# Performance work log

Hardware: AMD Instinct MI355X
Metric: run time of the kernel (lower is better)

Reference implementation:

```python
import jax, jax.numpy as jnp
import numpy as np

H_IMG, W_IMG = 256, 512      # image_size
P = 224                      # focus_patch_size
FS = 14                      # feature_size -> L = 196
DM = 384                     # d_model
POOL = P // FS               # 16


def _grid_sample_bilinear_zeros(img, grid):
    """torch F.grid_sample(mode='bilinear', padding_mode='zeros', align_corners=False).
    img: (B, C, H, W), grid: (B, Ho, Wo, 2) with (x, y) in [-1, 1]. -> (B, C, Ho, Wo)"""
    B, C, H, W = img.shape
    ix = (grid[..., 0] + 1.0) * (W * 0.5) - 0.5
    iy = (grid[..., 1] + 1.0) * (H * 0.5) - 0.5
    x0 = jnp.floor(ix); y0 = jnp.floor(iy)
    x1 = x0 + 1.0;      y1 = y0 + 1.0
    wx1 = ix - x0; wx0 = 1.0 - wx1
    wy1 = iy - y0; wy0 = 1.0 - wy1

    def gather(im, yy, xx):
        valid = ((xx >= 0) & (xx < W) & (yy >= 0) & (yy < H)).astype(im.dtype)
        xc = jnp.clip(xx, 0, W - 1).astype(jnp.int32)
        yc = jnp.clip(yy, 0, H - 1).astype(jnp.int32)
        return im[:, yc, xc] * valid[None]  # (C, Ho, Wo)

    def sample_one(im, x0, x1, y0, y1, wx0, wx1, wy0, wy1):
        return (gather(im, y0, x0) * (wy0 * wx0)[None]
                + gather(im, y0, x1) * (wy0 * wx1)[None]
                + gather(im, y1, x0) * (wy1 * wx0)[None]
                + gather(im, y1, x1) * (wy1 * wx1)[None])

    return jax.vmap(sample_one)(img, x0, x1, y0, y1, wx0, wx1, wy0, wy1)


def setup_inputs() -> dict:
    key = jax.random.key(0)
    ks = jax.random.split(key, 9)
    B = 128
    images = jax.random.normal(ks[0], (B, 3, H_IMG, W_IMG), jnp.float32)
    positions = jax.random.uniform(ks[1], (B, 2), jnp.float32)          # (x, y) in [0,1]
    global_features = jax.random.normal(ks[2], (B, FS * FS, DM), jnp.float32)
    Wp = jax.random.normal(ks[3], (3, DM), jnp.float32) * 0.1           # focus_net stand-in proj
    bp = jnp.zeros((DM,), jnp.float32)
    w1 = jax.random.normal(ks[4], (DM, DM // 4), jnp.float32) * 0.05    # fusion-weight MLP
    b1 = jnp.zeros((DM // 4,), jnp.float32)
    w2 = jax.random.normal(ks[5], (DM // 4, 1), jnp.float32) * 0.05
    b2 = jnp.zeros((1,), jnp.float32)
    return dict(images=images, positions=positions, global_features=global_features,
                Wp=Wp, bp=bp, w1=w1, b1=b1, w2=w2, b2=b2, seq_len=1)


def reference(images, positions, global_features, Wp, bp, w1, b1, w2, b2, seq_len):
    B = images.shape[0]
    L = FS * FS
    # ---- get_img_patches: wraparound crop (vectorized over batch) ----
    px = jnp.clip(positions[:, 0], 0.0, 1.0)
    py = jnp.clip(positions[:, 1], 0.0, 1.0)
    x_start = (jnp.trunc(px * W_IMG - P / 2).astype(jnp.int32)) % W_IMG           # int() then % W
    y_start = jnp.floor(jnp.clip(py * H_IMG - P / 2, 0.0, H_IMG - P)).astype(jnp.int32)
    xi = (x_start[:, None] + jnp.arange(P)[None, :]) % W_IMG                      # (B, P) wraparound
    yi = y_start[:, None] + jnp.arange(P)[None, :]                                # (B, P)
    patches = jax.vmap(lambda im, y, x: im[:, y][:, :, x])(images, yi, xi)        # (B, 3, P, P)

    # affine_grid(theta, (1,1,FS,FS), align_corners=False)
    xs = x_start.astype(jnp.float32)
    ys = y_start.astype(jnp.float32)
    u = ((jnp.arange(FS, dtype=jnp.float32) + 0.5) * 2.0 / FS) - 1.0              # base grid coords
    gx = (P / W_IMG) * u[None, None, :] + ((2.0 * xs + P) / W_IMG - 1.0)[:, None, None]
    gy = (P / H_IMG) * u[None, :, None] + ((2.0 * ys + P) / H_IMG - 1.0)[:, None, None]
    grid = jnp.stack([jnp.broadcast_to(gx, (B, FS, FS)),
                      jnp.broadcast_to(gy, (B, FS, FS))], axis=-1)                # (B, FS, FS, 2)

    # ---- focus_net stand-in: 16x16 avg-pool + linear 3 -> d_model ----
    pooled = patches.reshape(B, 3, FS, POOL, FS, POOL).mean(axis=(3, 5))          # (B, 3, FS, FS)
    local = jnp.einsum('bchw,cd->bhwd', pooled, Wp) + bp                          # (B, FS, FS, DM)
    local_features = local.reshape(B, L, DM)

    # ---- update_global_features: grid_sample scatter + gated update ----
    local_2d = local.transpose(0, 3, 1, 2)                                        # (B, DM, FS, FS)
    fw = jax.nn.sigmoid(jnp.einsum('blk,ko->blo',
                                   jax.nn.gelu(jnp.einsum('blc,ch->blh', local_features, w1) + b1),
                                   w2) + b2)                                      # (B, L, 1)
    sampled = _grid_sample_bilinear_zeros(local_2d, grid)                         # (B, DM, FS, FS)
    sampled = sampled.transpose(0, 2, 3, 1).reshape(B, L, DM)
    updated = global_features + fw * sampled                                      # broadcast expand
    return updated
```

## Files before the change

kernel.cpp:

```cpp
#include <hip/hip_runtime.h>
#include <math.h>

#define H_IMG 256
#define W_IMG 512
#define PSZ   224
#define FS    14
#define L     196
#define DM    384
#define HID   96
#define TPB   32

__device__ __forceinline__ void get_starts(const float* __restrict__ pos, int b,
                                           int& xs, int& ys) {
    float px = pos[b * 2 + 0];
    float py = pos[b * 2 + 1];
    px = fminf(fmaxf(px, 0.0f), 1.0f);
    py = fminf(fmaxf(py, 0.0f), 1.0f);
    int xv = (int)truncf(px * (float)W_IMG - 112.0f);
    xs = ((xv % W_IMG) + W_IMG) % W_IMG;
    float yv = py * (float)H_IMG - 112.0f;
    yv = fminf(fmaxf(yv, 0.0f), (float)(H_IMG - PSZ));
    ys = (int)floorf(yv);
}

__global__ __launch_bounds__(256) void pool_pre_kernel(
    const float* __restrict__ img, const float* __restrict__ pos,
    const float* __restrict__ Wp,  const float* __restrict__ bp,
    const float* __restrict__ w1,  const float* __restrict__ b1,
    float* __restrict__ pooled, float* __restrict__ A, float* __restrict__ B0,
    int B)
{
    const int HW = H_IMG * W_IMG;
    int blk = blockIdx.x;
    int b = blk / FS;
    int i = blk % FS;
    int t = threadIdx.x;
    int xs, ys;
    get_starts(pos, b, xs, ys);

    if (t < PSZ) {
        int col = xs + t;
        if (col >= W_IMG) col -= W_IMG;
        int row0 = ys + i * 16;
        const float* ip = img + (size_t)b * 3 * HW + (size_t)row0 * W_IMG + col;
        float a0 = 0.f, a1 = 0.f, a2 = 0.f;
        #pragma unroll
        for (int dy = 0; dy < 16; ++dy) {
            const float* r = ip + dy * W_IMG;
            a0 += r[0];
            a1 += r[HW];
            a2 += r[2 * HW];
        }
        #pragma unroll
        for (int d = 1; d < 16; d <<= 1) {
            a0 += __shfl_xor(a0, d);
            a1 += __shfl_xor(a1, d);
            a2 += __shfl_xor(a2, d);
        }
        if ((t & 15) == 0) {
            int li = i * FS + (t >> 4);
            pooled[((size_t)b * 3 + 0) * L + li] = a0 * (1.0f / 256.0f);
            pooled[((size_t)b * 3 + 1) * L + li] = a1 * (1.0f / 256.0f);
            pooled[((size_t)b * 3 + 2) * L + li] = a2 * (1.0f / 256.0f);
        }
    }

    if (blk == 0 && t < HID) {
        float a0 = 0.f, a1 = 0.f, a2 = 0.f, ab = 0.f;
        #pragma unroll 4
        for (int d = 0; d < DM; ++d) {
            float w = w1[d * HID + t];
            a0 += Wp[0 * DM + d] * w;
            a1 += Wp[1 * DM + d] * w;
            a2 += Wp[2 * DM + d] * w;
            ab += bp[d] * w;
        }
        A[0 * HID + t] = a0;
        A[1 * HID + t] = a1;
        A[2 * HID + t] = a2;
        B0[t] = ab + b1[t];
    }
}

__global__ __launch_bounds__(256) void fused_update_kernel(
    const float* __restrict__ pos, const float* __restrict__ pooled,
    const float* __restrict__ A,   const float* __restrict__ B0,
    const float* __restrict__ w2,  const float* __restrict__ b2,
    const float* __restrict__ gf,  const float* __restrict__ Wp,
    const float* __restrict__ bp,  float* __restrict__ out, int B)
{
    __shared__ float  sA[3 * HID];
    __shared__ float  sB0[HID];
    __shared__ float  sw2[HID];
    __shared__ float4 sWp4[3 * DM / 4];
    __shared__ float4 sbp4[DM / 4];
    __shared__ float  sMeta[TPB][5];

    int tid = threadIdx.x;
    if (tid < 3 * HID) sA[tid] = A[tid];
    if (tid < HID) { sB0[tid] = B0[tid]; sw2[tid] = w2[tid]; }
    {
        if (tid < 288) sWp4[tid] = ((const float4*)Wp)[tid];
        if (tid < 96)  sbp4[tid] = ((const float4*)bp)[tid];
    }
    __syncthreads();

    const int nTok = B * L;
    int bt = blockIdx.x * TPB;
    int g = tid >> 3;
    int s = tid & 7;
    int token = bt + g;
    if (token >= nTok) token = nTok - 1;
    int b = token / L;
    int l = token % L;

    const float* pb = pooled + (size_t)b * 3 * L;
    float p0 = pb[l], p1 = pb[L + l], p2 = pb[2 * L + l];

    float acc = 0.0f;
    #pragma unroll
    for (int m = 0; m < 12; ++m) {
        int k = s + 8 * m;
        float x = sB0[k] + p0 * sA[k] + p1 * sA[HID + k] + p2 * sA[2 * HID + k];
        float e = __expf(1.5957691216057308f * (x + 0.044715f * x * x * x));
        float th = 1.0f - 2.0f / (e + 1.0f);
        acc += 0.5f * x * (1.0f + th) * sw2[k];
    }
    acc += __shfl_xor(acc, 1);
    acc += __shfl_xor(acc, 2);
    acc += __shfl_xor(acc, 4);

    if (s == 0) {
        float fw = 1.0f / (1.0f + __expf(-(acc + b2[0])));

        int xs, ys;
        get_starts(pos, b, xs, ys);
        int i = l / FS, j = l % FS;
        float uj = ((j + 0.5f) * 2.0f) / 14.0f - 1.0f;
        float ui = ((i + 0.5f) * 2.0f) / 14.0f - 1.0f;
        float gx = (224.0f / 512.0f) * uj + ((2.0f * (float)xs + 224.0f) / 512.0f - 1.0f);
        float gy = (224.0f / 256.0f) * ui + ((2.0f * (float)ys + 224.0f) / 256.0f - 1.0f);
        float ix = (gx + 1.0f) * 7.0f - 0.5f;
        float iy = (gy + 1.0f) * 7.0f - 0.5f;
        float x0f = floorf(ix), y0f = floorf(iy);
        float wx1 = ix - x0f, wx0 = 1.0f - wx1;
        float wy1 = iy - y0f, wy0 = 1.0f - wy1;
        int x0 = (int)x0f, y0 = (int)y0f;
        int x1 = x0 + 1, y1 = y0 + 1;

        float ps0 = 0.f, ps1 = 0.f, ps2 = 0.f, wsum = 0.f;
        const int   cx[4] = { x0, x1, x0, x1 };
        const int   cy[4] = { y0, y0, y1, y1 };
        const float cw[4] = { wy0 * wx0, wy0 * wx1, wy1 * wx0, wy1 * wx1 };
        #pragma unroll
        for (int n = 0; n < 4; ++n) {
            int X = cx[n], Y = cy[n];
            if (X >= 0 && X < FS && Y >= 0 && Y < FS) {
                float w = cw[n];
                int li = Y * FS + X;
                ps0 += w * pb[li];
                ps1 += w * pb[L + li];
                ps2 += w * pb[2 * L + li];
                wsum += w;
            }
        }
        sMeta[g][0] = fw;  sMeta[g][1] = wsum;
        sMeta[g][2] = ps0; sMeta[g][3] = ps1; sMeta[g][4] = ps2;
    }
    __syncthreads();

    const float4* gf4  = (const float4*)gf  + (size_t)bt * (DM / 4);
    float4*       out4 = (float4*)out       + (size_t)bt * (DM / 4);
    long long maxItem = (long long)(nTok - bt) * (DM / 4);
    #pragma unroll
    for (int it = 0; it < 12; ++it) {
        int item = it * 256 + tid;
        if (item >= maxItem) break;
        int tl = item / (DM / 4);
        int d4 = item - tl * (DM / 4);
        float fw   = sMeta[tl][0];
        float wsum = sMeta[tl][1];
        float ps0  = sMeta[tl][2];
        float ps1  = sMeta[tl][3];
        float ps2  = sMeta[tl][4];
        float4 g4 = gf4[item];
        float4 w0 = sWp4[d4];
        float4 w1v = sWp4[96 + d4];
        float4 w2v = sWp4[192 + d4];
        float4 bv = sbp4[d4];
        float4 o;
        o.x = g4.x + fw * (wsum * bv.x + ps0 * w0.x + ps1 * w1v.x + ps2 * w2v.x);
        o.y = g4.y + fw * (wsum * bv.y + ps0 * w0.y + ps1 * w1v.y + ps2 * w2v.y);
        o.z = g4.z + fw * (wsum * bv.z + ps0 * w0.z + ps1 * w1v.z + ps2 * w2v.z);
        o.w = g4.w + fw * (wsum * bv.w + ps0 * w0.w + ps1 * w1v.w + ps2 * w2v.w);
        out4[item] = o;
    }
}

extern "C" void kernel_launch(void* const* d_in, const int* in_sizes, int n_in,
                              void* d_out, int out_size, void* d_ws, size_t ws_size,
                              hipStream_t stream) {
    const float* images    = (const float*)d_in[0];
    const float* positions = (const float*)d_in[1];
    const float* gf        = (const float*)d_in[2];
    const float* Wp        = (const float*)d_in[3];
    const float* bp        = (const float*)d_in[4];
    const float* w1        = (const float*)d_in[5];
    const float* b1        = (const float*)d_in[6];
    const float* w2        = (const float*)d_in[7];
    const float* b2        = (const float*)d_in[8];

    const int B = in_sizes[1] / 2;

    float* ws = (float*)d_ws;
    float* pooled = ws;
    float* A      = ws + (size_t)B * 3 * L;
    float* B0     = A + 3 * HID;

    hipLaunchKernelGGL(pool_pre_kernel, dim3(B * FS), dim3(256), 0, stream,
                       images, positions, Wp, bp, w1, b1, pooled, A, B0, B);

    int nTok = B * L;
    hipLaunchKernelGGL(fused_update_kernel, dim3((nTok + TPB - 1) / TPB), dim3(256), 0, stream,
                       positions, pooled, A, B0, w2, b2, gf, Wp, bp, (float*)d_out, B);
}
```

Measured before the change: 59.91 us.

## Fuse pooling, gating MLP and update into a single per-half-image kernel

After: 128.4 us. 2.14x slower.

```diff
diff --git a/kernel.cpp b/kernel.cpp
--- a/kernel.cpp
+++ b/kernel.cpp
@@ -3,179 +3,157 @@
 
 #define H_IMG 256
 #define W_IMG 512
-#define PSZ   224
 #define FS    14
 #define L     196
 #define DM    384
 #define HID   96
-#define TPB   32
 
-__device__ __forceinline__ void get_starts(const float* __restrict__ pos, int b,
-                                           int& xs, int& ys) {
-    float px = pos[b * 2 + 0];
-    float py = pos[b * 2 + 1];
-    px = fminf(fmaxf(px, 0.0f), 1.0f);
-    py = fminf(fmaxf(py, 0.0f), 1.0f);
-    int xv = (int)truncf(px * (float)W_IMG - 112.0f);
-    xs = ((xv % W_IMG) + W_IMG) % W_IMG;
-    float yv = py * (float)H_IMG - 112.0f;
-    yv = fminf(fmaxf(yv, 0.0f), (float)(H_IMG - PSZ));
-    ys = (int)floorf(yv);
-}
+__global__ __launch_bounds__(512) void fused_all_kernel(
+    const float* __restrict__ img, const float* __restrict__ pos,
+    const float* __restrict__ gf,  const float* __restrict__ Wp,
+    const float* __restrict__ bp,  const float* __restrict__ w1,
+    const float* __restrict__ b1,  const float* __restrict__ w2,
+    const float* __restrict__ b2,  float* __restrict__ out, int B)
+{
+    __shared__ float  sPool[3][8][FS];
+    __shared__ float  sA[3 * HID];
+    __shared__ float  sB0[HID];
+    __shared__ float  sw2v[HID];
+    __shared__ float4 sWp4[3 * DM / 4];
+    __shared__ float4 sbp4[DM / 4];
+    __shared__ float  sMeta[98][5];
 
-__global__ __launch_bounds__(256) void pool_pre_kernel(
-    const float* __restrict__ img, const float* __restrict__ pos,
-    const float* __restrict__ Wp,  const float* __restrict__ bp,
-    const float* __restrict__ w1,  const float* __restrict__ b1,
-    float* __restrict__ pooled, float* __restrict__ A, float* __restrict__ B0,
-    int B)
-{
     const int HW = H_IMG * W_IMG;
-    int blk = blockIdx.x;
-    int b = blk / FS;
-    int i = blk % FS;
-    int t = threadIdx.x;
-    int xs, ys;
-    get_starts(pos, b, xs, ys);
+    const int tid  = threadIdx.x;
+    const int blk  = blockIdx.x;
+    const int b    = blk >> 1;
+    const int half = blk & 1;
+    const int rbase = 6 * half;
 
-    if (t < PSZ) {
-        int col = xs + t;
-        if (col >= W_IMG) col -= W_IMG;
-        int row0 = ys + i * 16;
-        const float* ip = img + (size_t)b * 3 * HW + (size_t)row0 * W_IMG + col;
-        float a0 = 0.f, a1 = 0.f, a2 = 0.f;
+    if (tid < 288)       sWp4[tid]        = ((const float4*)Wp)[tid];
+    else if (tid < 384)  sbp4[tid - 288]  = ((const float4*)bp)[tid - 288];
+    else if (tid < 480)  sw2v[tid - 384]  = w2[tid - 384];
+    float b2v = b2[0];
+
+    float px = fminf(fmaxf(pos[2 * b + 0], 0.f), 1.f);
+    float py = fminf(fmaxf(pos[2 * b + 1], 0.f), 1.f);
+    int xs = ((int)truncf(px * 512.f - 112.f)) % 512; if (xs < 0) xs += 512;
+    float yv = fminf(fmaxf(py * 256.f - 112.f, 0.f), 32.f);
+    int ys = (int)floorf(yv);
+
+    if (tid < 448) {
+        int ct   = tid % 224;
+        int ihalf = tid / 224;
+        int col = xs + ct; if (col >= W_IMG) col -= W_IMG;
+        const float* ipb = img + (size_t)b * 3 * HW + col;
         #pragma unroll
-        for (int dy = 0; dy < 16; ++dy) {
-            const float* r = ip + dy * W_IMG;
-            a0 += r[0];
-            a1 += r[HW];
-            a2 += r[2 * HW];
+        for (int ii = 0; ii < 4; ++ii) {
+            int il = ii * 2 + ihalf;
+            int row0 = ys + (rbase + il) * 16;
+            const float* ip = ipb + (size_t)row0 * W_IMG;
+            float a0 = 0.f, a1 = 0.f, a2 = 0.f;
+            #pragma unroll
+            for (int dy = 0; dy < 16; ++dy) {
+                const float* r = ip + dy * W_IMG;
+                a0 += r[0];
+                a1 += r[HW];
+                a2 += r[2 * HW];
+            }
+            #pragma unroll
+            for (int d = 1; d < 16; d <<= 1) {
+                a0 += __shfl_xor(a0, d);
+                a1 += __shfl_xor(a1, d);
+                a2 += __shfl_xor(a2, d);
+            }
+            if ((tid & 15) == 0) {
+                int pc = ct >> 4;
+                sPool[0][il][pc] = a0 * (1.f / 256.f);
+                sPool[1][il][pc] = a1 * (1.f / 256.f);
+                sPool[2][il][pc] = a2 * (1.f / 256.f);
+            }
         }
-        #pragma unroll
-        for (int d = 1; d < 16; d <<= 1) {
-            a0 += __shfl_xor(a0, d);
-            a1 += __shfl_xor(a1, d);
-            a2 += __shfl_xor(a2, d);
-        }
-        if ((t & 15) == 0) {
-            int li = i * FS + (t >> 4);
-            pooled[((size_t)b * 3 + 0) * L + li] = a0 * (1.0f / 256.0f);
-            pooled[((size_t)b * 3 + 1) * L + li] = a1 * (1.0f / 256.0f);
-            pooled[((size_t)b * 3 + 2) * L + li] = a2 * (1.0f / 256.0f);
-        }
-    }
-
-    if (blk == 0 && t < HID) {
+    } else {
+        int k = tid - 448;
         float a0 = 0.f, a1 = 0.f, a2 = 0.f, ab = 0.f;
+        float c0 = 0.f, c1 = 0.f, c2 = 0.f, cb = 0.f;
         #pragma unroll 4
         for (int d = 0; d < DM; ++d) {
-            float w = w1[d * HID + t];
-            a0 += Wp[0 * DM + d] * w;
-            a1 += Wp[1 * DM + d] * w;
-            a2 += Wp[2 * DM + d] * w;
-            ab += bp[d] * w;
+            float wv  = w1[d * HID + k];
+            float w0r = Wp[d], w1r = Wp[DM + d], w2r = Wp[2 * DM + d], bpr = bp[d];
+            a0 += w0r * wv; a1 += w1r * wv; a2 += w2r * wv; ab += bpr * wv;
+            if (k < 32) {
+                float wv2 = w1[d * HID + k + 64];
+                c0 += w0r * wv2; c1 += w1r * wv2; c2 += w2r * wv2; cb += bpr * wv2;
+            }
         }
-        A[0 * HID + t] = a0;
-        A[1 * HID + t] = a1;
-        A[2 * HID + t] = a2;
-        B0[t] = ab + b1[t];
-    }
-}
-
-__global__ __launch_bounds__(256) void fused_update_kernel(
-    const float* __restrict__ pos, const float* __restrict__ pooled,
-    const float* __restrict__ A,   const float* __restrict__ B0,
-    const float* __restrict__ w2,  const float* __restrict__ b2,
-    const float* __restrict__ gf,  const float* __restrict__ Wp,
-    const float* __restrict__ bp,  float* __restrict__ out, int B)
-{
-    __shared__ float  sA[3 * HID];
-    __shared__ float  sB0[HID];
-    __shared__ float  sw2[HID];
-    __shared__ float4 sWp4[3 * DM / 4];
-    __shared__ float4 sbp4[DM / 4];
-    __shared__ float  sMeta[TPB][5];
-
-    int tid = threadIdx.x;
-    if (tid < 3 * HID) sA[tid] = A[tid];
-    if (tid < HID) { sB0[tid] = B0[tid]; sw2[tid] = w2[tid]; }
-    {
-        if (tid < 288) sWp4[tid] = ((const float4*)Wp)[tid];
-        if (tid < 96)  sbp4[tid] = ((const float4*)bp)[tid];
+        sA[k] = a0; sA[HID + k] = a1; sA[2 * HID + k] = a2; sB0[k] = ab + b1[k];
+        if (k < 32) {
+            sA[k + 64] = c0; sA[HID + k + 64] = c1; sA[2 * HID + k + 64] = c2;
+            sB0[k + 64] = cb + b1[k + 64];
+        }
     }
     __syncthreads();
 
-    const int nTok = B * L;
-    int bt = blockIdx.x * TPB;
-    int g = tid >> 3;
-    int s = tid & 7;
-    int token = bt + g;
-    if (token >= nTok) token = nTok - 1;
-    int b = token / L;
-    int l = token % L;
+    if (tid < 392) {
+        int g = tid >> 2, s = tid & 3;
+        int il = g / FS, j = g - il * FS;
+        int i  = half * 7 + il;
+        int lrow = il + half;
+        float p0 = sPool[0][lrow][j];
+        float p1 = sPool[1][lrow][j];
+        float p2 = sPool[2][lrow][j];
 
-    const float* pb = pooled + (size_t)b * 3 * L;
-    float p0 = pb[l], p1 = pb[L + l], p2 = pb[2 * L + l];
+        float acc = 0.f;
+        #pragma unroll
+        for (int m = 0; m < 24; ++m) {
+            int k = s + 4 * m;
+            float x = sB0[k] + p0 * sA[k] + p1 * sA[HID + k] + p2 * sA[2 * HID + k];
+            float e = __expf(1.5957691216057308f * (x + 0.044715f * x * x * x));
+            float th = 1.f - 2.f / (e + 1.f);
+            acc += 0.5f * x * (1.f + th) * sw2v[k];
+        }
+        acc += __shfl_xor(acc, 1);
+        acc += __shfl_xor(acc, 2);
 
-    float acc = 0.0f;
-    #pragma unroll
-    for (int m = 0; m < 12; ++m) {
-        int k = s + 8 * m;
-        float x = sB0[k] + p0 * sA[k] + p1 * sA[HID + k] + p2 * sA[2 * HID + k];
-        float e = __expf(1.5957691216057308f * (x + 0.044715f * x * x * x));
-        float th = 1.0f - 2.0f / (e + 1.0f);
-        acc += 0.5f * x * (1.0f + th) * sw2[k];
-    }
-    acc += __shfl_xor(acc, 1);
-    acc += __shfl_xor(acc, 2);
-    acc += __shfl_xor(acc, 4);
+        if (s == 0) {
+            float fw = 1.f / (1.f + __expf(-(acc + b2v)));
 
-    if (s == 0) {
-        float fw = 1.0f / (1.0f + __expf(-(acc + b2[0])));
+            float uj = ((j + 0.5f) * 2.f) / 14.f - 1.f;
+            float ui = ((i + 0.5f) * 2.f) / 14.f - 1.f;
+            float gx = (224.f / 512.f) * uj + ((2.f * (float)xs + 224.f) / 512.f - 1.f);
+            float gy = (224.f / 256.f) * ui + ((2.f * (float)ys + 224.f) / 256.f - 1.f);
+            float ix = (gx + 1.f) * 7.f - 0.5f;
+            float iy = (gy + 1.f) * 7.f - 0.5f;
+            float x0f = floorf(ix), y0f = floorf(iy);
+            float wx1 = ix - x0f, wx0 = 1.f - wx1;
+            float wy1 = iy - y0f, wy0 = 1.f - wy1;
+            int x0 = (int)x0f, y0 = (int)y0f, x1 = x0 + 1, y1 = y0 + 1;
 
-        int xs, ys;
-        get_starts(pos, b, xs, ys);
-        int i = l / FS, j = l % FS;
-        float uj = ((j + 0.5f) * 2.0f) / 14.0f - 1.0f;
-        float ui = ((i + 0.5f) * 2.0f) / 14.0f - 1.0f;
-        float gx = (224.0f / 512.0f) * uj + ((2.0f * (float)xs + 224.0f) / 512.0f - 1.0f);
-        float gy = (224.0f / 256.0f) * ui + ((2.0f * (float)ys + 224.0f) / 256.0f - 1.0f);
-        float ix = (gx + 1.0f) * 7.0f - 0.5f;
-        float iy = (gy + 1.0f) * 7.0f - 0.5f;
-        float x0f = floorf(ix), y0f = floorf(iy);
-        float wx1 = ix - x0f, wx0 = 1.0f - wx1;
-        float wy1 = iy - y0f, wy0 = 1.0f - wy1;
-        int x0 = (int)x0f, y0 = (int)y0f;
-        int x1 = x0 + 1, y1 = y0 + 1;
-
-        float ps0 = 0.f, ps1 = 0.f, ps2 = 0.f, wsum = 0.f;
-        const int   cx[4] = { x0, x1, x0, x1 };
-        const int   cy[4] = { y0, y0, y1, y1 };
-        const float cw[4] = { wy0 * wx0, wy0 * wx1, wy1 * wx0, wy1 * wx1 };
-        #pragma unroll
-        for (int n = 0; n < 4; ++n) {
-            int X = cx[n], Y = cy[n];
-            if (X >= 0 && X < FS && Y >= 0 && Y < FS) {
-                float w = cw[n];
-                int li = Y * FS + X;
-                ps0 += w * pb[li];
-                ps1 += w * pb[L + li];
-                ps2 += w * pb[2 * L + li];
-                wsum += w;
+            float ps0 = 0.f, ps1 = 0.f, ps2 = 0.f, wsum = 0.f;
+            const int   cx[4] = { x0, x1, x0, x1 };
+            const int   cy[4] = { y0, y0, y1, y1 };
+            const float cw[4] = { wy0 * wx0, wy0 * wx1, wy1 * wx0, wy1 * wx1 };
+            #pragma unroll
+            for (int n = 0; n < 4; ++n) {
+                int X = cx[n], Y = cy[n], ly = Y - rbase;
+                if (X >= 0 && X < FS && Y >= 0 && Y < FS && ly >= 0 && ly < 8) {
+                    float w = cw[n];
+                    ps0 += w * sPool[0][ly][X];
+                    ps1 += w * sPool[1][ly][X];
+                    ps2 += w * sPool[2][ly][X];
+                    wsum += w;
+                }
             }
+            sMeta[g][0] = fw;  sMeta[g][1] = wsum;
+            sMeta[g][2] = ps0; sMeta[g][3] = ps1; sMeta[g][4] = ps2;
         }
-        sMeta[g][0] = fw;  sMeta[g][1] = wsum;
-        sMeta[g][2] = ps0; sMeta[g][3] = ps1; sMeta[g][4] = ps2;
     }
     __syncthreads();
 
-    const float4* gf4  = (const float4*)gf  + (size_t)bt * (DM / 4);
-    float4*       out4 = (float4*)out       + (size_t)bt * (DM / 4);
-    long long maxItem = (long long)(nTok - bt) * (DM / 4);
-    #pragma unroll
-    for (int it = 0; it < 12; ++it) {
-        int item = it * 256 + tid;
-        if (item >= maxItem) break;
+    size_t base4 = ((size_t)b * L + (size_t)half * 98) * (DM / 4);
+    const float4* gf4  = (const float4*)gf  + base4;
+    float4*       out4 = (float4*)out       + base4;
+    for (int item = tid; item < 98 * (DM / 4); item += 512) {
         int tl = item / (DM / 4);
         int d4 = item - tl * (DM / 4);
         float fw   = sMeta[tl][0];
@@ -184,15 +162,15 @@
         float ps1  = sMeta[tl][3];
         float ps2  = sMeta[tl][4];
         float4 g4 = gf4[item];
-        float4 w0 = sWp4[d4];
-        float4 w1v = sWp4[96 + d4];
-        float4 w2v = sWp4[192 + d4];
-        float4 bv = sbp4[d4];
+        float4 W0 = sWp4[d4];
+        float4 W1 = sWp4[96 + d4];
+        float4 W2 = sWp4[192 + d4];
+        float4 BV = sbp4[d4];
         float4 o;
-        o.x = g4.x + fw * (wsum * bv.x + ps0 * w0.x + ps1 * w1v.x + ps2 * w2v.x);
-        o.y = g4.y + fw * (wsum * bv.y + ps0 * w0.y + ps1 * w1v.y + ps2 * w2v.y);
-        o.z = g4.z + fw * (wsum * bv.z + ps0 * w0.z + ps1 * w1v.z + ps2 * w2v.z);
-        o.w = g4.w + fw * (wsum * bv.w + ps0 * w0.w + ps1 * w1v.w + ps2 * w2v.w);
+        o.x = g4.x + fw * (wsum * BV.x + ps0 * W0.x + ps1 * W1.x + ps2 * W2.x);
+        o.y = g4.y + fw * (wsum * BV.y + ps0 * W0.y + ps1 * W1.y + ps2 * W2.y);
+        o.z = g4.z + fw * (wsum * BV.z + ps0 * W0.z + ps1 * W1.z + ps2 * W2.z);
+        o.w = g4.w + fw * (wsum * BV.w + ps0 * W0.w + ps1 * W1.w + ps2 * W2.w);
         out4[item] = o;
     }
 }
@@ -212,15 +190,7 @@
 
     const int B = in_sizes[1] / 2;
 
-    float* ws = (float*)d_ws;
-    float* pooled = ws;
-    float* A      = ws + (size_t)B * 3 * L;
-    float* B0     = A + 3 * HID;
-
-    hipLaunchKernelGGL(pool_pre_kernel, dim3(B * FS), dim3(256), 0, stream,
-                       images, positions, Wp, bp, w1, b1, pooled, A, B0, B);
-
-    int nTok = B * L;
-    hipLaunchKernelGGL(fused_update_kernel, dim3((nTok + TPB - 1) / TPB), dim3(256), 0, stream,
-                       positions, pooled, A, B0, w2, b2, gf, Wp, bp, (float*)d_out, B);
+    hipLaunchKernelGGL(fused_all_kernel, dim3(2 * B), dim3(512), 0, stream,
+                       images, positions, gf, Wp, bp, w1, b1, w2, b2,
+                       (float*)d_out, B);
 }
```
